# Performance work log

Measured on AMD Instinct MI355X. Metric: run time of the kernel, lower is better.

Reference implementation:

```python
import jax, jax.numpy as jnp
import numpy as np

B, N, D, H = 2, 2048, 1024, 16
d = D // H

def setup_inputs() -> dict:
    key = jax.random.key(0)
    k1, k2, k3, k4 = jax.random.split(key, 4)
    s = 1.0 / np.sqrt(D)
    return {
        "x": jax.random.normal(k1, (B, N, D), dtype=jnp.float32),
        "W_qk": jax.random.uniform(k2, (D, D), dtype=jnp.float32, minval=-s, maxval=s),
        "W_v": jax.random.uniform(k3, (D, D), dtype=jnp.float32, minval=-s, maxval=s),
        "W_out": jax.random.uniform(k4, (D, D), dtype=jnp.float32, minval=-s, maxval=s),
    }

def reference(x, W_qk, W_v, W_out):
    # tied Q=K projection; torch Linear computes x @ W.T
    qk = jnp.einsum('bnd,ed->bne', x, W_qk)          # (B,N,D)
    v = jnp.einsum('bnd,ed->bne', x, W_v)            # (B,N,D)
    qk = qk.reshape(B, N, H, d).transpose(0, 2, 1, 3)  # (B,H,N,d)
    v = v.reshape(B, N, H, d).transpose(0, 2, 1, 3)    # (B,H,N,d)
    dot = jnp.einsum('bhnd,bhmd->bhnm', qk, qk)      # (B,H,N,N)
    q2 = jnp.sum(qk * qk, axis=-1)                   # (B,H,N)
    logits = 2.0 * dot - q2[..., :, None] - q2[..., None, :]  # -||qi-qj||^2
    attn = jax.nn.softmax(logits, axis=-1)
    w = jnp.einsum('bhnm,bhmd->bhnd', attn, v)       # (B,H,N,d)
    out = w.transpose(0, 2, 1, 3).reshape(B, N, D)   # (B,N,D)
    return jnp.einsum('bnd,ed->bne', out, W_out)
```

## Files before the change

kernel.cpp:

```cpp
#include <hip/hip_runtime.h>

typedef __attribute__((ext_vector_type(8))) short short8;
typedef __attribute__((ext_vector_type(4))) float f32x4;
typedef __attribute__((ext_vector_type(16))) float f32x16;
typedef __attribute__((ext_vector_type(4))) unsigned short ushort4v;
typedef __attribute__((ext_vector_type(4))) unsigned int uint4v;
typedef __attribute__((ext_vector_type(2))) unsigned int uint2v;

constexpr int Nc = 2048, Kc = 1024;
constexpr float LOG2E = 1.4426950408889634f;

__device__ inline unsigned short f2bf(float f) {
  unsigned u = __builtin_bit_cast(unsigned, f);
  u = u + 0x7FFFu + ((u >> 16) & 1u);
  return (unsigned short)(u >> 16);
}
__device__ inline float bf2f(unsigned short h) {
  unsigned u = ((unsigned)h) << 16;
  return __builtin_bit_cast(float, u);
}
__device__ inline float fexp2(float x) {
  float r;
  asm("v_exp_f32 %0, %1" : "=v"(r) : "v"(x));
  return r;
}
__device__ inline unsigned cvt_pk_bf16(float lo, float hi) {
  unsigned r;
  asm("v_cvt_pk_bf16_f32 %0, %1, %2" : "=v"(r) : "v"(lo), "v"(hi));
  return r;
}

__device__ inline void gload_lds16(const void* g, void* l) {
  __builtin_amdgcn_global_load_lds(
      (const __attribute__((address_space(1))) unsigned int*)g,
      (__attribute__((address_space(3))) unsigned int*)l, 16, 0, 0);
}

__global__ __launch_bounds__(256) void cvt_bf16(const float* __restrict__ src,
                                                unsigned short* __restrict__ dst, int n8) {
  int i = blockIdx.x * 256 + threadIdx.x;
  if (i >= n8) return;
  const float4* s = reinterpret_cast<const float4*>(src) + 2 * (size_t)i;
  float4 a = s[0], b = s[1];
  short8 o;
  o[0] = (short)f2bf(a.x); o[1] = (short)f2bf(a.y); o[2] = (short)f2bf(a.z); o[3] = (short)f2bf(a.w);
  o[4] = (short)f2bf(b.x); o[5] = (short)f2bf(b.y); o[6] = (short)f2bf(b.z); o[7] = (short)f2bf(b.w);
  *reinterpret_cast<short8*>(dst + (size_t)i * 8) = o;
}

__global__ __launch_bounds__(256) void gemm_proj(const unsigned short* __restrict__ A,
                                                 const unsigned short* __restrict__ Wqk,
                                                 const unsigned short* __restrict__ Wv,
                                                 unsigned short* __restrict__ qk_out,
                                                 unsigned short* __restrict__ vt_out) {
  __shared__ unsigned short As[128 * 64];
  __shared__ unsigned short Bs[128 * 64];
  const int tid = threadIdx.x;
  const int bm = blockIdx.x & 31;
  const int bn = blockIdx.x >> 5;
  const bool isV = bn >= 8;
  const int lane = tid & 63, wid = tid >> 6;
  const int wr = wid >> 1, wc = wid & 1;
  const int lr = lane & 15, lg = lane >> 4;

  f32x4 acc[4][4] = {};

  const unsigned short* Abase = A + (size_t)bm * 128 * Kc;
  const unsigned short* Wbase = (isV ? Wv + (size_t)(bn - 8) * 128 * Kc
                                     : Wqk + (size_t)bn * 128 * Kc);

  for (int kt = 0; kt < Kc / 64; ++kt) {
    __syncthreads();
#pragma unroll
    for (int r = 0; r < 4; ++r) {
      int idx = r * 256 + tid;
      int row = idx >> 3, cc = idx & 7;
      int cs = cc ^ (row & 7);
      gload_lds16(Abase + (size_t)row * Kc + kt * 64 + cs * 8, &As[(r * 256 + wid * 64) * 8]);
      gload_lds16(Wbase + (size_t)row * Kc + kt * 64 + cs * 8, &Bs[(r * 256 + wid * 64) * 8]);
    }
    __syncthreads();

    short8 af[4][2], bfv[4][2];
#pragma unroll
    for (int m = 0; m < 4; ++m) {
      int row = wr * 64 + m * 16 + lr;
#pragma unroll
      for (int kh = 0; kh < 2; ++kh) {
        int cs = (kh * 4 + lg) ^ (row & 7);
        af[m][kh] = *reinterpret_cast<const short8*>(&As[row * 64 + cs * 8]);
      }
    }
#pragma unroll
    for (int n = 0; n < 4; ++n) {
      int row = wc * 64 + n * 16 + lr;
#pragma unroll
      for (int kh = 0; kh < 2; ++kh) {
        int cs = (kh * 4 + lg) ^ (row & 7);
        bfv[n][kh] = *reinterpret_cast<const short8*>(&Bs[row * 64 + cs * 8]);
      }
    }
#pragma unroll
    for (int kh = 0; kh < 2; ++kh)
#pragma unroll
      for (int m = 0; m < 4; ++m)
#pragma unroll
        for (int n = 0; n < 4; ++n)
          acc[m][n] = __builtin_amdgcn_mfma_f32_16x16x32_bf16(af[m][kh], bfv[n][kh], acc[m][n], 0, 0, 0);
  }

#pragma unroll
  for (int m = 0; m < 4; ++m) {
#pragma unroll
    for (int n = 0; n < 4; ++n) {
      int grow0 = bm * 128 + wr * 64 + m * 16 + lg * 4;
      int b = grow0 >> 11, nn0 = grow0 & 2047;
      if (isV) {
        int gcol = (bn - 8) * 128 + wc * 64 + n * 16 + lr;
        int h = gcol >> 6, dd = gcol & 63;
        ushort4v pk;
#pragma unroll
        for (int r = 0; r < 4; ++r) pk[r] = f2bf(acc[m][n][r]);
        *reinterpret_cast<ushort4v*>(&vt_out[(((size_t)(b * 16 + h)) * 64 + dd) * 2048 + nn0]) = pk;
      } else {
        int gcol = bn * 128 + wc * 64 + n * 16 + lr;
        int h = gcol >> 6, dd = gcol & 63;
#pragma unroll
        for (int r = 0; r < 4; ++r)
          qk_out[(((size_t)(b * 16 + h)) * 2048 + nn0 + r) * 64 + dd] = f2bf(acc[m][n][r]);
      }
    }
  }
}

__global__ __launch_bounds__(256) void gemm_out(const unsigned short* __restrict__ A,
                                                const unsigned short* __restrict__ W,
                                                float* __restrict__ out) {
  __shared__ unsigned short As[128 * 64];
  __shared__ unsigned short Bs[64 * 64];
  const int tid = threadIdx.x;
  const int bm = blockIdx.x & 31;
  const int bn = blockIdx.x >> 5;
  const int lane = tid & 63, wid = tid >> 6;
  const int wr = wid >> 1, wc = wid & 1;
  const int lr = lane & 15, lg = lane >> 4;

  f32x4 acc[4][2] = {};

  const unsigned short* Abase = A + (size_t)bm * 128 * Kc;
  const unsigned short* Wbase = W + (size_t)bn * 64 * Kc;

  for (int kt = 0; kt < Kc / 64; ++kt) {
    __syncthreads();
#pragma unroll
    for (int r = 0; r < 4; ++r) {
      int idx = r * 256 + tid;
      int row = idx >> 3, cc = idx & 7;
      int cs = cc ^ (row & 7);
      gload_lds16(Abase + (size_t)row * Kc + kt * 64 + cs * 8, &As[(r * 256 + wid * 64) * 8]);
    }
#pragma unroll
    for (int r = 0; r < 2; ++r) {
      int idx = r * 256 + tid;
      int row = idx >> 3, cc = idx & 7;
      int cs = cc ^ (row & 7);
      gload_lds16(Wbase + (size_t)row * Kc + kt * 64 + cs * 8, &Bs[(r * 256 + wid * 64) * 8]);
    }
    __syncthreads();

    short8 af[4][2], bfv[2][2];
#pragma unroll
    for (int m = 0; m < 4; ++m) {
      int row = wr * 64 + m * 16 + lr;
#pragma unroll
      for (int kh = 0; kh < 2; ++kh) {
        int cs = (kh * 4 + lg) ^ (row & 7);
        af[m][kh] = *reinterpret_cast<const short8*>(&As[row * 64 + cs * 8]);
      }
    }
#pragma unroll
    for (int n = 0; n < 2; ++n) {
      int row = wc * 32 + n * 16 + lr;
#pragma unroll
      for (int kh = 0; kh < 2; ++kh) {
        int cs = (kh * 4 + lg) ^ (row & 7);
        bfv[n][kh] = *reinterpret_cast<const short8*>(&Bs[row * 64 + cs * 8]);
      }
    }
#pragma unroll
    for (int kh = 0; kh < 2; ++kh)
#pragma unroll
      for (int m = 0; m < 4; ++m)
#pragma unroll
        for (int n = 0; n < 2; ++n)
          acc[m][n] = __builtin_amdgcn_mfma_f32_16x16x32_bf16(af[m][kh], bfv[n][kh], acc[m][n], 0, 0, 0);
  }

#pragma unroll
  for (int m = 0; m < 4; ++m)
#pragma unroll
    for (int n = 0; n < 2; ++n)
#pragma unroll
      for (int r = 0; r < 4; ++r) {
        int grow = bm * 128 + wr * 64 + m * 16 + lg * 4 + r;
        int gcol = bn * 64 + wc * 32 + n * 16 + lr;
        out[(size_t)grow * 1024 + gcol] = acc[m][n][r];
      }
}

__global__ __launch_bounds__(256) void q2_kernel(const unsigned short* __restrict__ qk,
                                                 float* __restrict__ q2l) {
  int t = blockIdx.x * 256 + threadIdx.x;
  int row = t >> 2, q = t & 3;
  const short8* p = reinterpret_cast<const short8*>(qk + (size_t)row * 64 + q * 16);
  short8 v0 = p[0], v1 = p[1];
  float s = 0.f;
#pragma unroll
  for (int i = 0; i < 8; ++i) {
    float f0 = bf2f((unsigned short)v0[i]);
    float f1 = bf2f((unsigned short)v1[i]);
    s += f0 * f0 + f1 * f1;
  }
  s += __shfl_xor(s, 1);
  s += __shfl_xor(s, 2);
  if (q == 0) q2l[row] = s * LOG2E;
}

template<bool PARTIAL>
__global__ __launch_bounds__(256) void attn_kernel(const unsigned short* __restrict__ qk,
                                                   const unsigned short* __restrict__ vt,
                                                   const float* __restrict__ q2lg_,
                                                   unsigned short* __restrict__ wout,
                                                   float* __restrict__ numP,
                                                   float* __restrict__ denP) {
  __shared__ unsigned short Ks[2][64 * 64];
  __shared__ unsigned short Vs[2][64 * 64];
  __shared__ float q2L[2][64];

  const int tid = threadIdx.x;
  const int chunk = PARTIAL ? 64 : 32;
  const int orig = (blockIdx.x & 7) * chunk + (blockIdx.x >> 3);
  const int half = PARTIAL ? (orig >> 8) : 0;
  const int rest = PARTIAL ? (orig & 255) : orig;
  const int bh = rest >> 3;
  const int qt = rest & 7;
  const int b = bh >> 4, h = bh & 15;
  const unsigned short* Qg = qk + (size_t)bh * Nc * 64;
  const unsigned short* Vg = vt + (size_t)bh * 64 * Nc;
  const float* q2lg = q2lg_ + (size_t)bh * Nc;
  const int lane = tid & 63, wid = tid >> 6;
  const int lo = lane & 31, hi = lane >> 5;

  const int qbase = qt * 256 + wid * 64;
  const int kt0 = half * 16;
  const int ktn = PARTIAL ? 16 : 32;

  short8 qf0[4], qf1[4];
#pragma unroll
  for (int kk = 0; kk < 4; ++kk) {
    qf0[kk] = *reinterpret_cast<const short8*>(
        Qg + (size_t)(qbase + lo) * 64 + kk * 16 + hi * 8);
    qf1[kk] = *reinterpret_cast<const short8*>(
        Qg + (size_t)(qbase + 32 + lo) * 64 + kk * 16 + hi * 8);
  }
  const float q2l_r0 = q2lg[qbase + lo];
  const float q2l_r1 = q2lg[qbase + 32 + lo];

  uint4v ou; ou[0] = 0x3F803F80u; ou[1] = 0x3F803F80u; ou[2] = 0x3F803F80u; ou[3] = 0x3F803F80u;
  const short8 ones = __builtin_bit_cast(short8, ou);

  f32x16 w00 = {}, w01 = {}, w10 = {}, w11 = {}, d0 = {}, d1 = {};

  auto stage = [&](int kt, int s) {
#pragma unroll
    for (int r = 0; r < 2; ++r) {
      int idx = r * 256 + tid;
      int row = idx >> 3, cc = idx & 7;
      int cs = cc ^ (row & 7);
      gload_lds16(Qg + (size_t)(kt * 64 + row) * 64 + cs * 8,
                  &Ks[s][(r * 256 + wid * 64) * 8]);
      gload_lds16(Vg + (size_t)row * Nc + kt * 64 + cs * 8,
                  &Vs[s][(r * 256 + wid * 64) * 8]);
    }
    if (tid < 16) gload_lds16(q2lg + kt * 64 + tid * 4, &q2L[s][0]);
  };

  stage(kt0, 0);
  __syncthreads();

  for (int t = 0; t < ktn; ++t) {
    const int kt = kt0 + t;
    const int cur = t & 1;
    if (t + 1 < ktn) stage(kt + 1, cur ^ 1);

#pragma unroll
    for (int kg = 0; kg < 2; ++kg) {
      short8 kf[4];
#pragma unroll
      for (int kk = 0; kk < 4; ++kk) {
        int row = kg * 32 + lo;
        int c = (kk * 2 + hi) ^ (row & 7);
        kf[kk] = *reinterpret_cast<const short8*>(&Ks[cur][row * 64 + c * 8]);
      }
      f32x16 s0 = {}, s1 = {};
      __builtin_amdgcn_s_setprio(1);
#pragma unroll
      for (int kk = 0; kk < 4; ++kk) {
        s0 = __builtin_amdgcn_mfma_f32_32x32x16_bf16(kf[kk], qf0[kk], s0, 0, 0, 0);
        s1 = __builtin_amdgcn_mfma_f32_32x32x16_bf16(kf[kk], qf1[kk], s1, 0, 0, 0);
      }
      __builtin_amdgcn_s_setprio(0);

      unsigned pk0[8], pk1[8];
#pragma unroll
      for (int q = 0; q < 4; ++q) {
        float4 k2q = *reinterpret_cast<const float4*>(&q2L[cur][kg * 32 + q * 8 + hi * 4]);
        float g0[4], g1[4];
#pragma unroll
        for (int rr = 0; rr < 4; ++rr) {
          int reg = q * 4 + rr;
          float k2 = (rr == 0) ? k2q.x : (rr == 1) ? k2q.y : (rr == 2) ? k2q.z : k2q.w;
          g0[rr] = fexp2(fmaf(s0[reg], 2.0f * LOG2E, -(q2l_r0 + k2)));
          g1[rr] = fexp2(fmaf(s1[reg], 2.0f * LOG2E, -(q2l_r1 + k2)));
        }
        pk0[q * 2]     = cvt_pk_bf16(g0[0], g0[1]);
        pk0[q * 2 + 1] = cvt_pk_bf16(g0[2], g0[3]);
        pk1[q * 2]     = cvt_pk_bf16(g1[0], g1[1]);
        pk1[q * 2 + 1] = cvt_pk_bf16(g1[2], g1[3]);
      }

#pragma unroll
      for (int kkl = 0; kkl < 2; ++kkl) {
        uint2v r00 = __builtin_amdgcn_permlane32_swap(pk0[4 * kkl + 0], pk0[4 * kkl + 2], false, false);
        uint2v r01 = __builtin_amdgcn_permlane32_swap(pk0[4 * kkl + 1], pk0[4 * kkl + 3], false, false);
        uint2v r10 = __builtin_amdgcn_permlane32_swap(pk1[4 * kkl + 0], pk1[4 * kkl + 2], false, false);
        uint2v r11 = __builtin_amdgcn_permlane32_swap(pk1[4 * kkl + 1], pk1[4 * kkl + 3], false, false);
        uint4v u0; u0[0] = r00[0]; u0[1] = r01[0]; u0[2] = r00[1]; u0[3] = r01[1];
        uint4v u1; u1[0] = r10[0]; u1[1] = r11[0]; u1[2] = r10[1]; u1[3] = r11[1];
        short8 pa0 = __builtin_bit_cast(short8, u0);
        short8 pa1 = __builtin_bit_cast(short8, u1);

        __builtin_amdgcn_s_setprio(1);
        d0 = __builtin_amdgcn_mfma_f32_32x32x16_bf16(pa0, ones, d0, 0, 0, 0);
        d1 = __builtin_amdgcn_mfma_f32_32x32x16_bf16(pa1, ones, d1, 0, 0, 0);
#pragma unroll
        for (int dt = 0; dt < 2; ++dt) {
          int row = dt * 32 + lo;
          int c = (kg * 4 + kkl * 2 + hi) ^ (row & 7);
          short8 vfr = *reinterpret_cast<const short8*>(&Vs[cur][row * 64 + c * 8]);
          if (dt == 0) {
            w00 = __builtin_amdgcn_mfma_f32_32x32x16_bf16(pa0, vfr, w00, 0, 0, 0);
            w10 = __builtin_amdgcn_mfma_f32_32x32x16_bf16(pa1, vfr, w10, 0, 0, 0);
          } else {
            w01 = __builtin_amdgcn_mfma_f32_32x32x16_bf16(pa0, vfr, w01, 0, 0, 0);
            w11 = __builtin_amdgcn_mfma_f32_32x32x16_bf16(pa1, vfr, w11, 0, 0, 0);
          }
        }
        __builtin_amdgcn_s_setprio(0);
      }
    }
    __syncthreads();
  }

  if constexpr (PARTIAL) {
    float* numh = numP + (size_t)half * 65536 * 64;
    float* denh = denP + (size_t)half * 65536;
#pragma unroll
    for (int reg = 0; reg < 16; ++reg) {
      int crow = (reg & 3) + 8 * (reg >> 2) + 4 * hi;
      size_t row0 = (size_t)bh * Nc + qbase + crow;
      size_t row1 = row0 + 32;
      numh[row0 * 64 + lo]      = w00[reg];
      numh[row0 * 64 + 32 + lo] = w01[reg];
      numh[row1 * 64 + lo]      = w10[reg];
      numh[row1 * 64 + 32 + lo] = w11[reg];
      if (lo == 0) { denh[row0] = d0[reg]; denh[row1] = d1[reg]; }
    }
  } else {
#pragma unroll
    for (int reg = 0; reg < 16; ++reg) {
      int crow = (reg & 3) + 8 * (reg >> 2) + 4 * hi;
      float iv0 = __builtin_amdgcn_rcpf(d0[reg]);
      float iv1 = __builtin_amdgcn_rcpf(d1[reg]);
      size_t base0 = ((size_t)b * Nc + qbase + crow) * 1024 + h * 64 + lo;
      size_t base1 = ((size_t)b * Nc + qbase + 32 + crow) * 1024 + h * 64 + lo;
      wout[base0]      = f2bf(w00[reg] * iv0);
      wout[base0 + 32] = f2bf(w01[reg] * iv0);
      wout[base1]      = f2bf(w10[reg] * iv1);
      wout[base1 + 32] = f2bf(w11[reg] * iv1);
    }
  }
}

__global__ __launch_bounds__(256) void combine_kernel(const float* __restrict__ numP,
                                                      const float* __restrict__ denP,
                                                      unsigned short* __restrict__ wout) {
  int gid = blockIdx.x * 256 + threadIdx.x;
  int row = gid >> 3, d0 = (gid & 7) * 8;
  const float* n0 = numP + (size_t)row * 64 + d0;
  const float* n1 = numP + (size_t)65536 * 64 + (size_t)row * 64 + d0;
  float iv = 1.0f / (denP[row] + denP[65536 + row]);
  float4 a0 = *reinterpret_cast<const float4*>(n0);
  float4 a1 = *reinterpret_cast<const float4*>(n0 + 4);
  float4 b0 = *reinterpret_cast<const float4*>(n1);
  float4 b1 = *reinterpret_cast<const float4*>(n1 + 4);
  short8 o;
  o[0] = (short)f2bf((a0.x + b0.x) * iv);
  o[1] = (short)f2bf((a0.y + b0.y) * iv);
  o[2] = (short)f2bf((a0.z + b0.z) * iv);
  o[3] = (short)f2bf((a0.w + b0.w) * iv);
  o[4] = (short)f2bf((a1.x + b1.x) * iv);
  o[5] = (short)f2bf((a1.y + b1.y) * iv);
  o[6] = (short)f2bf((a1.z + b1.z) * iv);
  o[7] = (short)f2bf((a1.w + b1.w) * iv);
  int bh = row >> 11, nn = row & 2047;
  int b = bh >> 4, h = bh & 15;
  *reinterpret_cast<short8*>(&wout[((size_t)b * Nc + nn) * 1024 + h * 64 + d0]) = o;
}

extern "C" void kernel_launch(void* const* d_in, const int* in_sizes, int n_in,
                              void* d_out, int out_size, void* d_ws, size_t ws_size,
                              hipStream_t stream) {
  const float* x    = (const float*)d_in[0];
  const float* Wqk  = (const float*)d_in[1];
  const float* Wv   = (const float*)d_in[2];
  const float* Wout = (const float*)d_in[3];
  float* out = (float*)d_out;
  char* ws = (char*)d_ws;

  unsigned short* x_bf    = (unsigned short*)(ws + 0);
  unsigned short* wqk_bf  = (unsigned short*)(ws + 8388608);
  unsigned short* wv_bf   = (unsigned short*)(ws + 10485760);
  unsigned short* wout_bf = (unsigned short*)(ws + 12582912);
  unsigned short* qk_buf  = (unsigned short*)(ws + 14680064);
  unsigned short* vt_buf  = (unsigned short*)(ws + 23068672);
  float*          q2l_buf = (float*)        (ws + 31457280);
  unsigned short* w_buf   = (unsigned short*)(ws + 31719424);
  float*          num_buf = (float*)        (ws + 40108032);
  float*          den_buf = (float*)        (ws + 73662464);
  const size_t need_split = 74186752;

  cvt_bf16<<<2048, 256, 0, stream>>>(x, x_bf, 524288);
  cvt_bf16<<<512, 256, 0, stream>>>(Wqk, wqk_bf, 131072);
  cvt_bf16<<<512, 256, 0, stream>>>(Wv, wv_bf, 131072);
  cvt_bf16<<<512, 256, 0, stream>>>(Wout, wout_bf, 131072);

  gemm_proj<<<512, 256, 0, stream>>>(x_bf, wqk_bf, wv_bf, qk_buf, vt_buf);

  q2_kernel<<<1024, 256, 0, stream>>>(qk_buf, q2l_buf);

  if (ws_size >= need_split) {
    attn_kernel<true><<<512, 256, 0, stream>>>(qk_buf, vt_buf, q2l_buf, nullptr, num_buf, den_buf);
    combine_kernel<<<2048, 256, 0, stream>>>(num_buf, den_buf, w_buf);
  } else {
    attn_kernel<false><<<256, 256, 0, stream>>>(qk_buf, vt_buf, q2l_buf, w_buf, nullptr, nullptr);
  }

  gemm_out<<<512, 256, 0, stream>>>(w_buf, wout_bf, out);
}
```

Measured before the change: 120.6 us.

## Fuse conversions and q2, split attention four ways with bf16 partials

Merges the four fp32-to-bf16 conversion launches into one kernel and computes the squared row norms inside the projection GEMM epilogue, removing the separate q2 pass. Attention now splits keys across four partitions and accumulates the softmax denominator with scalar adds in place of an extra MFMA against a ones vector. Partial numerators are stored as packed bf16, halving partial-buffer traffic, and the combine kernel sums four partials. This adds some precision loss in the partials and more combine reads, in exchange for more parallelism and fewer launches.

```diff
diff --git a/kernel.cpp b/kernel.cpp
--- a/kernel.cpp
+++ b/kernel.cpp
@@ -36,10 +36,27 @@
       (__attribute__((address_space(3))) unsigned int*)l, 16, 0, 0);
 }
 
-__global__ __launch_bounds__(256) void cvt_bf16(const float* __restrict__ src,
-                                                unsigned short* __restrict__ dst, int n8) {
-  int i = blockIdx.x * 256 + threadIdx.x;
-  if (i >= n8) return;
+__global__ __launch_bounds__(256) void cvt_all(const float* __restrict__ x,
+                                               const float* __restrict__ wqk,
+                                               const float* __restrict__ wv,
+                                               const float* __restrict__ wo,
+                                               unsigned short* __restrict__ xb,
+                                               unsigned short* __restrict__ wqkb,
+                                               unsigned short* __restrict__ wvb,
+                                               unsigned short* __restrict__ wob) {
+  int bid = blockIdx.x;
+  const float* src;
+  unsigned short* dst;
+  int i;
+  if (bid < 2048) {
+    src = x; dst = xb; i = bid * 256 + threadIdx.x;
+  } else {
+    int k = bid - 2048;
+    int which = k >> 9, sub = k & 511;
+    src = (which == 0) ? wqk : (which == 1) ? wv : wo;
+    dst = (which == 0) ? wqkb : (which == 1) ? wvb : wob;
+    i = sub * 256 + threadIdx.x;
+  }
   const float4* s = reinterpret_cast<const float4*>(src) + 2 * (size_t)i;
   float4 a = s[0], b = s[1];
   short8 o;
@@ -52,7 +69,8 @@
                                                  const unsigned short* __restrict__ Wqk,
                                                  const unsigned short* __restrict__ Wv,
                                                  unsigned short* __restrict__ qk_out,
-                                                 unsigned short* __restrict__ vt_out) {
+                                                 unsigned short* __restrict__ vt_out,
+                                                 float* __restrict__ q2l) {
   __shared__ unsigned short As[128 * 64];
   __shared__ unsigned short Bs[128 * 64];
   const int tid = threadIdx.x;
@@ -128,6 +146,28 @@
 #pragma unroll
         for (int r = 0; r < 4; ++r)
           qk_out[(((size_t)(b * 16 + h)) * 2048 + nn0 + r) * 64 + dd] = f2bf(acc[m][n][r]);
+      }
+    }
+  }
+
+  if (!isV) {
+    const int h = 2 * bn + wc;
+#pragma unroll
+    for (int m = 0; m < 4; ++m) {
+#pragma unroll
+      for (int r = 0; r < 4; ++r) {
+        float ss = 0.f;
+#pragma unroll
+        for (int n = 0; n < 4; ++n) ss += acc[m][n][r] * acc[m][n][r];
+        ss += __shfl_xor(ss, 1);
+        ss += __shfl_xor(ss, 2);
+        ss += __shfl_xor(ss, 4);
+        ss += __shfl_xor(ss, 8);
+        if (lr == 0) {
+          int grow = bm * 128 + wr * 64 + m * 16 + lg * 4 + r;
+          int b = grow >> 11, nn = grow & 2047;
+          q2l[((size_t)(b * 16 + h)) * 2048 + nn] = ss * LOG2E;
+        }
       }
     }
   }
@@ -208,37 +248,20 @@
       }
 }
 
-__global__ __launch_bounds__(256) void q2_kernel(const unsigned short* __restrict__ qk,
-                                                 float* __restrict__ q2l) {
-  int t = blockIdx.x * 256 + threadIdx.x;
-  int row = t >> 2, q = t & 3;
-  const short8* p = reinterpret_cast<const short8*>(qk + (size_t)row * 64 + q * 16);
-  short8 v0 = p[0], v1 = p[1];
-  float s = 0.f;
-#pragma unroll
-  for (int i = 0; i < 8; ++i) {
-    float f0 = bf2f((unsigned short)v0[i]);
-    float f1 = bf2f((unsigned short)v1[i]);
-    s += f0 * f0 + f1 * f1;
-  }
-  s += __shfl_xor(s, 1);
-  s += __shfl_xor(s, 2);
-  if (q == 0) q2l[row] = s * LOG2E;
-}
-
 template<bool PARTIAL>
-__global__ __launch_bounds__(256) void attn_kernel(const unsigned short* __restrict__ qk,
-                                                   const unsigned short* __restrict__ vt,
-                                                   const float* __restrict__ q2lg_,
-                                                   unsigned short* __restrict__ wout,
-                                                   float* __restrict__ numP,
-                                                   float* __restrict__ denP) {
+__global__ __launch_bounds__(256, 3) void attn_kernel(const unsigned short* __restrict__ qk,
+                                                      const unsigned short* __restrict__ vt,
+                                                      const float* __restrict__ q2lg_,
+                                                      unsigned short* __restrict__ wout,
+                                                      unsigned* __restrict__ num32,
+                                                      float* __restrict__ denP) {
   __shared__ unsigned short Ks[2][64 * 64];
   __shared__ unsigned short Vs[2][64 * 64];
   __shared__ float q2L[2][64];
+  __shared__ float invL[4][64];
 
   const int tid = threadIdx.x;
-  const int chunk = PARTIAL ? 64 : 32;
+  const int chunk = PARTIAL ? 128 : 32;
   const int orig = (blockIdx.x & 7) * chunk + (blockIdx.x >> 3);
   const int half = PARTIAL ? (orig >> 8) : 0;
   const int rest = PARTIAL ? (orig & 255) : orig;
@@ -252,8 +275,8 @@
   const int lo = lane & 31, hi = lane >> 5;
 
   const int qbase = qt * 256 + wid * 64;
-  const int kt0 = half * 16;
-  const int ktn = PARTIAL ? 16 : 32;
+  const int kt0 = half * 8;
+  const int ktn = PARTIAL ? 8 : 32;
 
   short8 qf0[4], qf1[4];
 #pragma unroll
@@ -266,10 +289,8 @@
   const float q2l_r0 = q2lg[qbase + lo];
   const float q2l_r1 = q2lg[qbase + 32 + lo];
 
-  uint4v ou; ou[0] = 0x3F803F80u; ou[1] = 0x3F803F80u; ou[2] = 0x3F803F80u; ou[3] = 0x3F803F80u;
-  const short8 ones = __builtin_bit_cast(short8, ou);
-
-  f32x16 w00 = {}, w01 = {}, w10 = {}, w11 = {}, d0 = {}, d1 = {};
+  f32x16 w00 = {}, w01 = {}, w10 = {}, w11 = {};
+  float den0 = 0.f, den1 = 0.f;
 
   auto stage = [&](int kt, int s) {
 #pragma unroll
@@ -302,47 +323,63 @@
         int c = (kk * 2 + hi) ^ (row & 7);
         kf[kk] = *reinterpret_cast<const short8*>(&Ks[cur][row * 64 + c * 8]);
       }
-      f32x16 s0 = {}, s1 = {};
-      __builtin_amdgcn_s_setprio(1);
-#pragma unroll
-      for (int kk = 0; kk < 4; ++kk) {
-        s0 = __builtin_amdgcn_mfma_f32_32x32x16_bf16(kf[kk], qf0[kk], s0, 0, 0, 0);
-        s1 = __builtin_amdgcn_mfma_f32_32x32x16_bf16(kf[kk], qf1[kk], s1, 0, 0, 0);
-      }
-      __builtin_amdgcn_s_setprio(0);
-
-      unsigned pk0[8], pk1[8];
-#pragma unroll
-      for (int q = 0; q < 4; ++q) {
-        float4 k2q = *reinterpret_cast<const float4*>(&q2L[cur][kg * 32 + q * 8 + hi * 4]);
-        float g0[4], g1[4];
-#pragma unroll
-        for (int rr = 0; rr < 4; ++rr) {
-          int reg = q * 4 + rr;
-          float k2 = (rr == 0) ? k2q.x : (rr == 1) ? k2q.y : (rr == 2) ? k2q.z : k2q.w;
-          g0[rr] = fexp2(fmaf(s0[reg], 2.0f * LOG2E, -(q2l_r0 + k2)));
-          g1[rr] = fexp2(fmaf(s1[reg], 2.0f * LOG2E, -(q2l_r1 + k2)));
+
+      unsigned pkA[8], pkB[8];
+      {
+        f32x16 s = {};
+        __builtin_amdgcn_s_setprio(1);
+#pragma unroll
+        for (int kk = 0; kk < 4; ++kk)
+          s = __builtin_amdgcn_mfma_f32_32x32x16_bf16(kf[kk], qf0[kk], s, 0, 0, 0);
+        __builtin_amdgcn_s_setprio(0);
+#pragma unroll
+        for (int q = 0; q < 4; ++q) {
+          float4 k2q = *reinterpret_cast<const float4*>(&q2L[cur][kg * 32 + q * 8 + hi * 4]);
+          float g[4];
+#pragma unroll
+          for (int rr = 0; rr < 4; ++rr) {
+            float k2 = (rr == 0) ? k2q.x : (rr == 1) ? k2q.y : (rr == 2) ? k2q.z : k2q.w;
+            g[rr] = fexp2(fmaf(s[q * 4 + rr], 2.0f * LOG2E, -(q2l_r0 + k2)));
+            den0 += g[rr];
+          }
+          pkA[q * 2]     = cvt_pk_bf16(g[0], g[1]);
+          pkA[q * 2 + 1] = cvt_pk_bf16(g[2], g[3]);
         }
-        pk0[q * 2]     = cvt_pk_bf16(g0[0], g0[1]);
-        pk0[q * 2 + 1] = cvt_pk_bf16(g0[2], g0[3]);
-        pk1[q * 2]     = cvt_pk_bf16(g1[0], g1[1]);
-        pk1[q * 2 + 1] = cvt_pk_bf16(g1[2], g1[3]);
+      }
+      {
+        f32x16 s = {};
+        __builtin_amdgcn_s_setprio(1);
+#pragma unroll
+        for (int kk = 0; kk < 4; ++kk)
+          s = __builtin_amdgcn_mfma_f32_32x32x16_bf16(kf[kk], qf1[kk], s, 0, 0, 0);
+        __builtin_amdgcn_s_setprio(0);
+#pragma unroll
+        for (int q = 0; q < 4; ++q) {
+          float4 k2q = *reinterpret_cast<const float4*>(&q2L[cur][kg * 32 + q * 8 + hi * 4]);
+          float g[4];
+#pragma unroll
+          for (int rr = 0; rr < 4; ++rr) {
+            float k2 = (rr == 0) ? k2q.x : (rr == 1) ? k2q.y : (rr == 2) ? k2q.z : k2q.w;
+            g[rr] = fexp2(fmaf(s[q * 4 + rr], 2.0f * LOG2E, -(q2l_r1 + k2)));
+            den1 += g[rr];
+          }
+          pkB[q * 2]     = cvt_pk_bf16(g[0], g[1]);
+          pkB[q * 2 + 1] = cvt_pk_bf16(g[2], g[3]);
+        }
       }
 
 #pragma unroll
       for (int kkl = 0; kkl < 2; ++kkl) {
-        uint2v r00 = __builtin_amdgcn_permlane32_swap(pk0[4 * kkl + 0], pk0[4 * kkl + 2], false, false);
-        uint2v r01 = __builtin_amdgcn_permlane32_swap(pk0[4 * kkl + 1], pk0[4 * kkl + 3], false, false);
-        uint2v r10 = __builtin_amdgcn_permlane32_swap(pk1[4 * kkl + 0], pk1[4 * kkl + 2], false, false);
-        uint2v r11 = __builtin_amdgcn_permlane32_swap(pk1[4 * kkl + 1], pk1[4 * kkl + 3], false, false);
+        uint2v r00 = __builtin_amdgcn_permlane32_swap(pkA[4 * kkl + 0], pkA[4 * kkl + 2], false, false);
+        uint2v r01 = __builtin_amdgcn_permlane32_swap(pkA[4 * kkl + 1], pkA[4 * kkl + 3], false, false);
+        uint2v r10 = __builtin_amdgcn_permlane32_swap(pkB[4 * kkl + 0], pkB[4 * kkl + 2], false, false);
+        uint2v r11 = __builtin_amdgcn_permlane32_swap(pkB[4 * kkl + 1], pkB[4 * kkl + 3], false, false);
         uint4v u0; u0[0] = r00[0]; u0[1] = r01[0]; u0[2] = r00[1]; u0[3] = r01[1];
         uint4v u1; u1[0] = r10[0]; u1[1] = r11[0]; u1[2] = r10[1]; u1[3] = r11[1];
         short8 pa0 = __builtin_bit_cast(short8, u0);
         short8 pa1 = __builtin_bit_cast(short8, u1);
 
         __builtin_amdgcn_s_setprio(1);
-        d0 = __builtin_amdgcn_mfma_f32_32x32x16_bf16(pa0, ones, d0, 0, 0, 0);
-        d1 = __builtin_amdgcn_mfma_f32_32x32x16_bf16(pa1, ones, d1, 0, 0, 0);
 #pragma unroll
         for (int dt = 0; dt < 2; ++dt) {
           int row = dt * 32 + lo;
@@ -362,26 +399,34 @@
     __syncthreads();
   }
 
+  den0 += __shfl_xor(den0, 32);
+  den1 += __shfl_xor(den1, 32);
+
   if constexpr (PARTIAL) {
-    float* numh = numP + (size_t)half * 65536 * 64;
+    unsigned* numh = num32 + (size_t)half * 65536 * 32;
     float* denh = denP + (size_t)half * 65536;
+    const int rowb = bh * Nc + qbase;
+    if (hi == 0) {
+      denh[rowb + lo] = den0;
+      denh[rowb + 32 + lo] = den1;
+    }
 #pragma unroll
     for (int reg = 0; reg < 16; ++reg) {
       int crow = (reg & 3) + 8 * (reg >> 2) + 4 * hi;
-      size_t row0 = (size_t)bh * Nc + qbase + crow;
-      size_t row1 = row0 + 32;
-      numh[row0 * 64 + lo]      = w00[reg];
-      numh[row0 * 64 + 32 + lo] = w01[reg];
-      numh[row1 * 64 + lo]      = w10[reg];
-      numh[row1 * 64 + 32 + lo] = w11[reg];
-      if (lo == 0) { denh[row0] = d0[reg]; denh[row1] = d1[reg]; }
+      numh[(size_t)(rowb + crow) * 32 + lo]      = cvt_pk_bf16(w00[reg], w01[reg]);
+      numh[(size_t)(rowb + 32 + crow) * 32 + lo] = cvt_pk_bf16(w10[reg], w11[reg]);
     }
   } else {
+    if (hi == 0) {
+      invL[wid][lo]      = __builtin_amdgcn_rcpf(den0);
+      invL[wid][32 + lo] = __builtin_amdgcn_rcpf(den1);
+    }
+    __syncthreads();
 #pragma unroll
     for (int reg = 0; reg < 16; ++reg) {
       int crow = (reg & 3) + 8 * (reg >> 2) + 4 * hi;
-      float iv0 = __builtin_amdgcn_rcpf(d0[reg]);
-      float iv1 = __builtin_amdgcn_rcpf(d1[reg]);
+      float iv0 = invL[wid][crow];
+      float iv1 = invL[wid][32 + crow];
       size_t base0 = ((size_t)b * Nc + qbase + crow) * 1024 + h * 64 + lo;
       size_t base1 = ((size_t)b * Nc + qbase + 32 + crow) * 1024 + h * 64 + lo;
       wout[base0]      = f2bf(w00[reg] * iv0);
@@ -392,30 +437,40 @@
   }
 }
 
-__global__ __launch_bounds__(256) void combine_kernel(const float* __restrict__ numP,
+__global__ __launch_bounds__(256) void combine_kernel(const unsigned* __restrict__ num32,
                                                       const float* __restrict__ denP,
                                                       unsigned short* __restrict__ wout) {
   int gid = blockIdx.x * 256 + threadIdx.x;
-  int row = gid >> 3, d0 = (gid & 7) * 8;
-  const float* n0 = numP + (size_t)row * 64 + d0;
-  const float* n1 = numP + (size_t)65536 * 64 + (size_t)row * 64 + d0;
-  float iv = 1.0f / (denP[row] + denP[65536 + row]);
-  float4 a0 = *reinterpret_cast<const float4*>(n0);
-  float4 a1 = *reinterpret_cast<const float4*>(n0 + 4);
-  float4 b0 = *reinterpret_cast<const float4*>(n1);
-  float4 b1 = *reinterpret_cast<const float4*>(n1 + 4);
-  short8 o;
-  o[0] = (short)f2bf((a0.x + b0.x) * iv);
-  o[1] = (short)f2bf((a0.y + b0.y) * iv);
-  o[2] = (short)f2bf((a0.z + b0.z) * iv);
-  o[3] = (short)f2bf((a0.w + b0.w) * iv);
-  o[4] = (short)f2bf((a1.x + b1.x) * iv);
-  o[5] = (short)f2bf((a1.y + b1.y) * iv);
-  o[6] = (short)f2bf((a1.z + b1.z) * iv);
-  o[7] = (short)f2bf((a1.w + b1.w) * iv);
+  int row = gid >> 2, quad = gid & 3;
+  float dsum = denP[row] + denP[65536 + row] + denP[131072 + row] + denP[196608 + row];
+  float iv = 1.0f / dsum;
+  float lo_[8] = {}, hi_[8] = {};
+#pragma unroll
+  for (int p = 0; p < 4; ++p) {
+    const uint4v* np = reinterpret_cast<const uint4v*>(
+        num32 + ((size_t)p * 65536 + row) * 32 + quad * 8);
+    uint4v a = np[0], c = np[1];
+#pragma unroll
+    for (int j = 0; j < 4; ++j) {
+      unsigned u = a[j];
+      lo_[j] += bf2f((unsigned short)(u & 0xffff));
+      hi_[j] += bf2f((unsigned short)(u >> 16));
+      unsigned v = c[j];
+      lo_[4 + j] += bf2f((unsigned short)(v & 0xffff));
+      hi_[4 + j] += bf2f((unsigned short)(v >> 16));
+    }
+  }
+  short8 o1, o2;
+#pragma unroll
+  for (int j = 0; j < 8; ++j) {
+    o1[j] = (short)f2bf(lo_[j] * iv);
+    o2[j] = (short)f2bf(hi_[j] * iv);
+  }
   int bh = row >> 11, nn = row & 2047;
   int b = bh >> 4, h = bh & 15;
-  *reinterpret_cast<short8*>(&wout[((size_t)b * Nc + nn) * 1024 + h * 64 + d0]) = o;
+  size_t base = ((size_t)b * Nc + nn) * 1024 + h * 64;
+  *reinterpret_cast<short8*>(&wout[base + quad * 8]) = o1;
+  *reinterpret_cast<short8*>(&wout[base + 32 + quad * 8]) = o2;
 }
 
 extern "C" void kernel_launch(void* const* d_in, const int* in_sizes, int n_in,
@@ -436,22 +491,17 @@
   unsigned short* vt_buf  = (unsigned short*)(ws + 23068672);
   float*          q2l_buf = (float*)        (ws + 31457280);
   unsigned short* w_buf   = (unsigned short*)(ws + 31719424);
-  float*          num_buf = (float*)        (ws + 40108032);
-  float*          den_buf = (float*)        (ws + 73662464);
-  const size_t need_split = 74186752;
-
-  cvt_bf16<<<2048, 256, 0, stream>>>(x, x_bf, 524288);
-  cvt_bf16<<<512, 256, 0, stream>>>(Wqk, wqk_bf, 131072);
-  cvt_bf16<<<512, 256, 0, stream>>>(Wv, wv_bf, 131072);
-  cvt_bf16<<<512, 256, 0, stream>>>(Wout, wout_bf, 131072);
-
-  gemm_proj<<<512, 256, 0, stream>>>(x_bf, wqk_bf, wv_bf, qk_buf, vt_buf);
-
-  q2_kernel<<<1024, 256, 0, stream>>>(qk_buf, q2l_buf);
+  unsigned*       num_buf = (unsigned*)     (ws + 40108032);
+  float*          den_buf = (float*)        (ws + 0);
+  const size_t need_split = 73662464;
+
+  cvt_all<<<3584, 256, 0, stream>>>(x, Wqk, Wv, Wout, x_bf, wqk_bf, wv_bf, wout_bf);
+
+  gemm_proj<<<512, 256, 0, stream>>>(x_bf, wqk_bf, wv_bf, qk_buf, vt_buf, q2l_buf);
 
   if (ws_size >= need_split) {
-    attn_kernel<true><<<512, 256, 0, stream>>>(qk_buf, vt_buf, q2l_buf, nullptr, num_buf, den_buf);
-    combine_kernel<<<2048, 256, 0, stream>>>(num_buf, den_buf, w_buf);
+    attn_kernel<true><<<1024, 256, 0, stream>>>(qk_buf, vt_buf, q2l_buf, nullptr, num_buf, den_buf);
+    combine_kernel<<<1024, 256, 0, stream>>>(num_buf, den_buf, w_buf);
   } else {
     attn_kernel<false><<<256, 256, 0, stream>>>(qk_buf, vt_buf, q2l_buf, w_buf, nullptr, nullptr);
   }
```

Result: slower. 153.5 us (+27.2%).
